# Kernel tuning notes

Measured on AMD Instinct MI355X. Metric: run time of the kernel, lower is better.

## Reference

```python
import jax, jax.numpy as jnp
import numpy as np

N_EL, N_NB, DIM = 8192, 24, 256
CUTOFF = 5.0
F0, F1 = 32, 16
N_ENV = 8
N_FEAT = 4  # [dist, dx, dy, dz]


def setup_inputs() -> dict:
    key = jax.random.key(0)
    ks = jax.random.split(key, 24)
    d = {}
    d['elec'] = jax.random.normal(ks[0], (N_EL, DIM), jnp.float32)
    d['msg'] = jax.random.normal(ks[1], (N_EL, DIM), jnp.float32)
    # positions inside a box of half the cutoff so pairs are within range
    d['r'] = jax.random.uniform(ks[2], (N_EL, 3), jnp.float32) * (0.5 * CUTOFF)
    d['r_nb'] = jax.random.uniform(ks[3], (N_EL, N_NB, 3), jnp.float32) * (0.5 * CUTOFF)
    d['s'] = jax.random.randint(ks[4], (N_EL,), 0, 2, jnp.int32)
    d['s_nb'] = jax.random.randint(ks[5], (N_EL, N_NB), 0, 2, jnp.int32)
    d['hinit_nb'] = jax.random.normal(ks[6], (N_EL, N_NB, DIM), jnp.float32)
    # parameters
    def lecun(k, shape):
        fan_in = shape[0]
        return jax.random.normal(k, shape, jnp.float32) / np.float32(np.sqrt(fan_in))
    d['W_in'] = lecun(ks[7], (DIM, DIM)); d['b_in'] = jnp.zeros((DIM,), jnp.float32)
    d['ee_scales'] = jax.random.uniform(ks[8], (N_ENV,), jnp.float32, 0.5, CUTOFF)
    d['ee_kernel'] = lecun(ks[9], (N_FEAT, F0))
    d['ee_bias'] = 2.0 * jax.random.normal(ks[10], (F0,), jnp.float32)
    d['Wf'] = lecun(ks[11], (F0 + N_ENV, F1)); d['bf'] = jnp.zeros((F1,), jnp.float32)
    d['Wsame'] = lecun(ks[12], (F1, DIM))
    d['Wdiff'] = lecun(ks[13], (F1, DIM))
    d['W1'] = lecun(ks[14], (DIM, DIM)); d['b1'] = jnp.zeros((DIM,), jnp.float32)
    d['W2'] = lecun(ks[15], (DIM, DIM)); d['b2'] = jnp.zeros((DIM,), jnp.float32)
    d['W3'] = lecun(ks[16], (DIM, DIM)); d['b3'] = jnp.zeros((DIM,), jnp.float32)
    d['scale'] = jnp.float32(1.0)  # FixedScalingFactor (identity at init)
    return d


def _forward(elec, msg, r, r_nb, s, s_nb, hinit_nb,
             W_in, b_in, ee_scales, ee_kernel, ee_bias, Wf, bf,
             Wsame, Wdiff, W1, b1, W2, b2, W3, b3, scale):
    silu = jax.nn.silu
    elec1 = silu(elec @ W_in + b_in)                       # [N, D]
    # get_diff_features: [dist, dx, dy, dz]
    diff = r_nb - r[:, None, :]                             # [N, K, 3]
    dist = jnp.sqrt(jnp.sum(diff * diff, -1) + 1e-12)       # [N, K]
    feats = jnp.concatenate([dist[..., None], diff], -1)    # [N, K, 4]
    spin_mask = s[:, None] == s_nb                          # [N, K]
    # PairwiseFilter: MLP on diff-features + radial envelopes, smooth cutoff
    env = jnp.exp(-jnp.square(dist[..., None] / ee_scales)) # [N, K, E]
    h = silu(feats @ ee_kernel + ee_bias)                   # [N, K, F0]
    h = jnp.concatenate([h, env], -1)                       # [N, K, F0+E]
    x = dist / CUTOFF
    cut = jnp.where(dist < CUTOFF, jnp.square(1.0 - x) * (1.0 + 2.0 * x), 0.0)
    beta = (h @ Wf + bf) * cut[..., None]                   # [N, K, F1]
    gamma = jnp.where(spin_mask[..., None], beta @ Wsame, beta @ Wdiff)  # [N, K, D]
    hinit_msg = jnp.einsum('nid,nid->nd', silu(elec1[:, None] + hinit_nb), gamma)
    out = silu(elec1 @ W1 + b1 + hinit_msg)
    out = silu(out @ W2 + b2 + msg)
    out = silu(out @ W3 + b3)
    return (out + elec1) * scale


def reference(elec, msg, r, r_nb, s, s_nb, hinit_nb,
              W_in, b_in, ee_scales, ee_kernel, ee_bias, Wf, bf,
              Wsame, Wdiff, W1, b1, W2, b2, W3, b3, scale):
    return _forward(elec, msg, r, r_nb, s, s_nb, hinit_nb,
                    W_in, b_in, ee_scales, ee_kernel, ee_bias, Wf, bf,
                    Wsame, Wdiff, W1, b1, W2, b2, W3, b3, scale)
```

## Files before the change

kernel.cpp:

```cpp
#include <hip/hip_runtime.h>

#define DIM 256
#define PDIM 260
#define PD2  264
#define SBPITCH 20
#define NNB 24
#define NEL 8192
#define ROWS 16
#define NT 1024
#define CUTOFF 5.0f

typedef unsigned int u32;
typedef unsigned short u16;
typedef __attribute__((ext_vector_type(8))) short bf16x8;
typedef __attribute__((ext_vector_type(4))) float f32x4;

__device__ __forceinline__ u16 f2b(float f){
  union{float f;u32 i;}v; v.f=f;
  u32 r = v.i + 0x7fffu + ((v.i>>16)&1u);
  return (u16)(r>>16);
}
__device__ __forceinline__ float b2f(u16 u){
  union{u32 i;float f;}v; v.i = ((u32)u)<<16; return v.f;
}
__device__ __forceinline__ float fast_silu(float x){
  float e = __builtin_amdgcn_exp2f(-1.44269504088896340f * x);
  return x * __builtin_amdgcn_rcpf(1.0f + e);
}

__global__ __launch_bounds__(256)
void wprep(const float* __restrict__ W0, const float* __restrict__ W1,
           const float* __restrict__ W2, const float* __restrict__ W3,
           const float* __restrict__ Wsame, const float* __restrict__ Wdiff,
           u16* __restrict__ ws){
  if (blockIdx.x < 1024){
    const int mat = blockIdx.x >> 8;
    const int n   = blockIdx.x & 255;
    const int k   = threadIdx.x;
    const float* W = (mat==0)?W0:(mat==1)?W1:(mat==2)?W2:W3;
    ws[(mat<<16) + (n<<8) + k] = f2b(W[(k<<8) + n]);
  } else {
    const int n = threadIdx.x;
    u16* dst = ws + 4*65536 + n*32;
    #pragma unroll
    for (int kk = 0; kk < 16; kk++){
      dst[kk]    = f2b(Wsame[kk*DIM + n]);
      dst[16+kk] = f2b(Wdiff[kk*DIM + n]);
    }
  }
}

template<int MODE, int ABF16>
__device__ __forceinline__ void gemm_mfma(
    const void* A, u16* sE1b, float* sR1,
    const u16* __restrict__ Wt, const float* __restrict__ bias,
    const float* __restrict__ extraGbl, float* __restrict__ outGbl,
    float scl, int n0, int t)
{
  const int lane = t & 63;
  const int ln   = lane & 15;
  const int quad = lane >> 4;
  const int w    = t >> 6;
  f32x4 acc = {0.f,0.f,0.f,0.f};
  const u16* bp = Wt + (w*16 + ln)*DIM;
  #pragma unroll
  for (int ks = 0; ks < 8; ks++){
    const int k0 = ks*32 + quad*8;
    bf16x8 af;
    if (ABF16){
      af = *(const bf16x8*)((const u16*)A + ln*PD2 + k0);
    } else {
      const float* arow = (const float*)A + ln*PDIM;
      float4 a01 = *(const float4*)(arow + k0);
      float4 a23 = *(const float4*)(arow + k0 + 4);
      af[0]=(short)f2b(a01.x); af[1]=(short)f2b(a01.y);
      af[2]=(short)f2b(a01.z); af[3]=(short)f2b(a01.w);
      af[4]=(short)f2b(a23.x); af[5]=(short)f2b(a23.y);
      af[6]=(short)f2b(a23.z); af[7]=(short)f2b(a23.w);
    }
    bf16x8 b0 = *(const bf16x8*)(bp + k0);
    acc = __builtin_amdgcn_mfma_f32_16x16x32_bf16(af, b0, acc, 0, 0, 0);
  }
  if (MODE == 2) __syncthreads();
  #pragma unroll
  for (int r = 0; r < 4; r++){
    const int m = quad*4 + r;
    const int n = w*16 + ln;
    float v = acc[r] + bias[n];
    if (MODE == 1) v += sR1[m*PDIM + n];
    if (MODE == 2) v += extraGbl[(size_t)(n0+m)*DIM + n];
    v = fast_silu(v);
    if (MODE == 0)      sE1b[m*PD2 + n] = f2b(v);
    else if (MODE == 3) outGbl[(size_t)(n0+m)*DIM + n] = (v + b2f(sE1b[m*PD2 + n])) * scl;
    else                sR1[m*PDIM + n] = v;
  }
}

__global__ __launch_bounds__(NT, 8)
void fused_moon_kernel(
    const float* __restrict__ elec, const float* __restrict__ msg,
    const float* __restrict__ rpos, const float* __restrict__ rnb,
    const int* __restrict__ s,    const int* __restrict__ snb,
    const float* __restrict__ hinit,
    const float* __restrict__ bin,
    const float* __restrict__ eesc, const float* __restrict__ eek,
    const float* __restrict__ eeb,  const float* __restrict__ Wf,
    const float* __restrict__ bfb,
    const float* __restrict__ b1, const float* __restrict__ b2,
    const float* __restrict__ b3,
    const float* __restrict__ scalep,
    const u16* __restrict__ Wt,
    float* __restrict__ out)
{
  __shared__ float sR1[ROWS*PDIM];
  __shared__ u16   sE1b[ROWS*PD2];
  __shared__ u16   sBC[NNB*16*SBPITCH];
  __shared__ u32   sMaskB[ROWS];
  const int t  = threadIdx.x;
  const int n0 = blockIdx.x * ROWS;

  if (t < ROWS) sMaskB[t] = 0u;
  {
    const float4* ep = (const float4*)elec;
    float4 v = ep[(size_t)n0*64 + t];
    *(float4*)&sR1[(t>>6)*PDIM + (t&63)*4] = v;
  }
  __syncthreads();

  gemm_mfma<0,0>(sR1, sE1b, sR1, Wt, bin, nullptr, nullptr, 0.f, n0, t);

  if (t < 2*ROWS*NNB) {
    const int half = t & 1;
    const int pr = t >> 1;
    const int rr = pr / NNB;
    const int k  = pr - rr*NNB;
    const int n  = n0 + rr;
    const float* rp  = rpos + n*3;
    const float* rnp = rnb + (n*NNB + k)*3;
    float dx = rnp[0] - rp[0];
    float dy = rnp[1] - rp[1];
    float dz = rnp[2] - rp[2];
    float dist = sqrtf(dx*dx + dy*dy + dz*dz + 1e-12f);
    float feats[4] = {dist, dx, dy, dz};
    float h[32];
    #pragma unroll
    for (int f4 = 0; f4 < 8; f4++){
      float4 a4 = *(const float4*)&eeb[4*f4];
      float av[4] = {a4.x, a4.y, a4.z, a4.w};
      #pragma unroll
      for (int i = 0; i < 4; i++){
        float4 kv = *(const float4*)&eek[i*32 + 4*f4];
        av[0]+=feats[i]*kv.x; av[1]+=feats[i]*kv.y; av[2]+=feats[i]*kv.z; av[3]+=feats[i]*kv.w;
      }
      h[4*f4+0]=fast_silu(av[0]); h[4*f4+1]=fast_silu(av[1]);
      h[4*f4+2]=fast_silu(av[2]); h[4*f4+3]=fast_silu(av[3]);
    }
    float env[8];
    #pragma unroll
    for (int e = 0; e < 8; e++){
      float q = dist * __builtin_amdgcn_rcpf(eesc[e]);
      env[e] = __builtin_amdgcn_exp2f(-1.44269504088896340f * q * q);
    }
    float xx = dist * (1.0f/CUTOFF);
    float cut = (dist < CUTOFF) ? (1.0f-xx)*(1.0f-xx)*(1.0f+2.0f*xx) : 0.0f;
    u16* rowp = &sBC[(k*16 + rr)*SBPITCH];
    #pragma unroll
    for (int jj = 0; jj < 2; jj++){
      const int j4 = half*2 + jj;
      float4 a4 = *(const float4*)&bfb[4*j4];
      float av[4] = {a4.x, a4.y, a4.z, a4.w};
      #pragma unroll
      for (int f = 0; f < 40; f++){
        float val = (f < 32) ? h[f] : env[f-32];
        float4 wv = *(const float4*)&Wf[f*16 + 4*j4];
        av[0]+=val*wv.x; av[1]+=val*wv.y; av[2]+=val*wv.z; av[3]+=val*wv.w;
      }
      ushort4 bv;
      bv.x = f2b(av[0]*cut); bv.y = f2b(av[1]*cut);
      bv.z = f2b(av[2]*cut); bv.w = f2b(av[3]*cut);
      *(ushort4*)(rowp + 4*j4) = bv;
    }
    if (half == 0 && s[n] == snb[n*NNB + k]) atomicOr(&sMaskB[rr], 1u << k);
  }
  __syncthreads();

  {
    const int lane = t & 63;
    const int ln   = lane & 15;
    const int quad = lane >> 4;
    const int w    = t >> 6;
    const int C0   = w << 4;
    const int nA   = C0 + (quad << 2);
    const u16* Wcat = Wt + 4*65536;
    bf16x8 bs0 = *(const bf16x8*)(Wcat + (C0 + ln)*32 + quad*8);

    float e1A[4];
    {
      ushort4 ea = *(const ushort4*)&sE1b[ln*PD2 + nA];
      e1A[0]=b2f(ea.x); e1A[1]=b2f(ea.y); e1A[2]=b2f(ea.z); e1A[3]=b2f(ea.w);
    }
    const u32 mb = sMaskB[ln];
    const float* hp = hinit + (size_t)(n0 + ln)*NNB*DIM + nA;
    float4 h0 = *(const float4*)(hp + 0*DIM);
    float4 h1 = *(const float4*)(hp + 1*DIM);
    float4 h2 = *(const float4*)(hp + 2*DIM);
    float4 h3 = *(const float4*)(hp + 3*DIM);
    float hmA[4] = {0.f,0.f,0.f,0.f};
    for (int k = 0; k < NNB; k++){
      const int kp = (k+4 < NNB) ? (k+4) : (NNB-1);
      float4 h4 = *(const float4*)(hp + kp*DIM);
      bf16x8 b8 = *(const bf16x8*)(&sBC[(k*16 + ln)*SBPITCH + (quad&1)*8]);
      const u16 km = (u16)((((u32)(quad>>1) ^ ((mb>>k)&1u)) != 0u) ? 0xFFFFu : 0u);
      bf16x8 af;
      #pragma unroll
      for (int j = 0; j < 8; j++) af[j] = (short)((u16)b8[j] & km);
      f32x4 z = {0.f,0.f,0.f,0.f};
      f32x4 g0 = __builtin_amdgcn_mfma_f32_16x16x32_bf16(bs0, af, z, 0, 0, 0);
      hmA[0] += fast_silu(e1A[0]+h0.x)*g0[0];
      hmA[1] += fast_silu(e1A[1]+h0.y)*g0[1];
      hmA[2] += fast_silu(e1A[2]+h0.z)*g0[2];
      hmA[3] += fast_silu(e1A[3]+h0.w)*g0[3];
      h0=h1; h1=h2; h2=h3; h3=h4;
    }
    *(float4*)&sR1[ln*PDIM + nA] = make_float4(hmA[0],hmA[1],hmA[2],hmA[3]);
  }
  __syncthreads();

  const float scl = scalep[0];

  gemm_mfma<1,1>(sE1b, sE1b, sR1, Wt + (1<<16), b1, nullptr, nullptr, 0.f, n0, t);
  __syncthreads();
  gemm_mfma<2,0>(sR1, sE1b, sR1, Wt + (2<<16), b2, msg, nullptr, 0.f, n0, t);
  __syncthreads();
  gemm_mfma<3,0>(sR1, sE1b, sR1, Wt + (3<<16), b3, nullptr, out, scl, n0, t);
}

extern "C" void kernel_launch(void* const* d_in, const int* in_sizes, int n_in,
                              void* d_out, int out_size, void* d_ws, size_t ws_size,
                              hipStream_t stream) {
  (void)in_sizes; (void)n_in; (void)ws_size; (void)out_size;
  const float* elec  = (const float*)d_in[0];
  const float* msg   = (const float*)d_in[1];
  const float* rpos  = (const float*)d_in[2];
  const float* rnb   = (const float*)d_in[3];
  const int*   s     = (const int*)d_in[4];
  const int*   snb   = (const int*)d_in[5];
  const float* hinit = (const float*)d_in[6];
  const float* Win   = (const float*)d_in[7];
  const float* bin   = (const float*)d_in[8];
  const float* eesc  = (const float*)d_in[9];
  const float* eek   = (const float*)d_in[10];
  const float* eeb   = (const float*)d_in[11];
  const float* Wf    = (const float*)d_in[12];
  const float* bfb   = (const float*)d_in[13];
  const float* Wsame = (const float*)d_in[14];
  const float* Wdiff = (const float*)d_in[15];
  const float* W1    = (const float*)d_in[16];
  const float* b1    = (const float*)d_in[17];
  const float* W2    = (const float*)d_in[18];
  const float* b2    = (const float*)d_in[19];
  const float* W3    = (const float*)d_in[20];
  const float* b3    = (const float*)d_in[21];
  const float* scl   = (const float*)d_in[22];
  float* outp        = (float*)d_out;
  u16*   wt          = (u16*)d_ws;

  wprep<<<dim3(1025), dim3(256), 0, stream>>>(Win, W1, W2, W3, Wsame, Wdiff, wt);
  fused_moon_kernel<<<dim3(NEL/ROWS), dim3(NT), 0, stream>>>(
      elec, msg, rpos, rnb, s, snb, hinit,
      bin, eesc, eek, eeb, Wf, bfb,
      b1, b2, b3, scl, wt, outp);
}
```

Before: 377.5 us.

## Stream hinit neighbor rows into double-buffered LDS via global_load_lds

Neighbor hidden states (hinit) are no longer loaded by each lane straight from global memory, where a wave touched 16 scattered rows with a four-deep register prefetch. Each wave now loads one whole row per neighbor into a two-slot LDS ring using direct global-to-LDS loads. The first two neighbors are issued at kernel start, and each later neighbor is issued behind barriers with explicit vmcnt waits. This gives fully coalesced global reads, at the cost of about 33 KB more LDS, a shallower prefetch and two workgroup barriers per neighbor iteration.

Result: slower. 385.2 us (+2.0%).

```diff
diff --git a/kernel.cpp b/kernel.cpp
--- a/kernel.cpp
+++ b/kernel.cpp
@@ -14,6 +14,10 @@
 typedef unsigned short u16;
 typedef __attribute__((ext_vector_type(8))) short bf16x8;
 typedef __attribute__((ext_vector_type(4))) float f32x4;
+
+#define GL_LDS(g, l) __builtin_amdgcn_global_load_lds( \
+    (const __attribute__((address_space(1))) void*)(g), \
+    (__attribute__((address_space(3))) void*)(l), 16, 0, 0)
 
 __device__ __forceinline__ u16 f2b(float f){
   union{float f;u32 i;}v; v.f=f;
@@ -116,8 +120,15 @@
   __shared__ u16   sE1b[ROWS*PD2];
   __shared__ u16   sBC[NNB*16*SBPITCH];
   __shared__ u32   sMaskB[ROWS];
+  __shared__ float sH[2][ROWS*PDIM];
   const int t  = threadIdx.x;
   const int n0 = blockIdx.x * ROWS;
+  const int lane = t & 63;
+  const int w    = t >> 6;
+
+  const float* hs = hinit + ((size_t)(n0 + w)*NNB)*DIM + (lane<<2);
+  GL_LDS(hs,        &sH[0][w*PDIM]);
+  GL_LDS(hs + DIM,  &sH[1][w*PDIM]);
 
   if (t < ROWS) sMaskB[t] = 0u;
   {
@@ -185,10 +196,8 @@
   __syncthreads();
 
   {
-    const int lane = t & 63;
     const int ln   = lane & 15;
     const int quad = lane >> 4;
-    const int w    = t >> 6;
     const int C0   = w << 4;
     const int nA   = C0 + (quad << 2);
     const u16* Wcat = Wt + 4*65536;
@@ -200,15 +209,9 @@
       e1A[0]=b2f(ea.x); e1A[1]=b2f(ea.y); e1A[2]=b2f(ea.z); e1A[3]=b2f(ea.w);
     }
     const u32 mb = sMaskB[ln];
-    const float* hp = hinit + (size_t)(n0 + ln)*NNB*DIM + nA;
-    float4 h0 = *(const float4*)(hp + 0*DIM);
-    float4 h1 = *(const float4*)(hp + 1*DIM);
-    float4 h2 = *(const float4*)(hp + 2*DIM);
-    float4 h3 = *(const float4*)(hp + 3*DIM);
     float hmA[4] = {0.f,0.f,0.f,0.f};
     for (int k = 0; k < NNB; k++){
-      const int kp = (k+4 < NNB) ? (k+4) : (NNB-1);
-      float4 h4 = *(const float4*)(hp + kp*DIM);
+      float4 hv = *(const float4*)&sH[k&1][ln*PDIM + nA];
       bf16x8 b8 = *(const bf16x8*)(&sBC[(k*16 + ln)*SBPITCH + (quad&1)*8]);
       const u16 km = (u16)((((u32)(quad>>1) ^ ((mb>>k)&1u)) != 0u) ? 0xFFFFu : 0u);
       bf16x8 af;
@@ -216,11 +219,20 @@
       for (int j = 0; j < 8; j++) af[j] = (short)((u16)b8[j] & km);
       f32x4 z = {0.f,0.f,0.f,0.f};
       f32x4 g0 = __builtin_amdgcn_mfma_f32_16x16x32_bf16(bs0, af, z, 0, 0, 0);
-      hmA[0] += fast_silu(e1A[0]+h0.x)*g0[0];
-      hmA[1] += fast_silu(e1A[1]+h0.y)*g0[1];
-      hmA[2] += fast_silu(e1A[2]+h0.z)*g0[2];
-      hmA[3] += fast_silu(e1A[3]+h0.w)*g0[3];
-      h0=h1; h1=h2; h2=h3; h3=h4;
+      hmA[0] += fast_silu(e1A[0]+hv.x)*g0[0];
+      hmA[1] += fast_silu(e1A[1]+hv.y)*g0[1];
+      hmA[2] += fast_silu(e1A[2]+hv.z)*g0[2];
+      hmA[3] += fast_silu(e1A[3]+hv.w)*g0[3];
+      __builtin_amdgcn_sched_barrier(0);
+      __builtin_amdgcn_s_barrier();
+      if (k + 2 < NNB){
+        GL_LDS(hs + (size_t)(k+2)*DIM, &sH[k&1][w*PDIM]);
+        asm volatile("s_waitcnt vmcnt(1)" ::: "memory");
+      } else {
+        asm volatile("s_waitcnt vmcnt(0)" ::: "memory");
+      }
+      __builtin_amdgcn_sched_barrier(0);
+      __builtin_amdgcn_s_barrier();
     }
     *(float4*)&sR1[ln*PDIM + nA] = make_float4(hmA[0],hmA[1],hmA[2],hmA[3]);
   }
```
